# Kernel tuning notes

Hardware: AMD Instinct MI355X
Metric: run time of the kernel (lower is better)

## Reference

```python
import jax, jax.numpy as jnp
import numpy as np

NUM_POINT = 9
BASE_SCALE = 8.0
STRIDE = 8.0


def setup_inputs() -> dict:
    key = jax.random.key(0)
    k1, k2, k3 = jax.random.split(key, 3)
    B, C, H, W = 2, 256, 100, 100
    N = H * W
    feat_map = jax.random.normal(k1, (B, C, H, W), dtype=jnp.float32)
    # grid of location centers (x, y, stride) like the anchor/center generator
    ys, xs = jnp.meshgrid(jnp.arange(H, dtype=jnp.float32), jnp.arange(W, dtype=jnp.float32), indexing='ij')
    cx = (xs.reshape(-1) + 0.5) * STRIDE
    cy = (ys.reshape(-1) + 0.5) * STRIDE
    locations = jnp.stack([cx, cy, jnp.full((N,), STRIDE, dtype=jnp.float32)], axis=-1)
    offset = jax.random.normal(k2, (B, N, NUM_POINT, 2), dtype=jnp.float32) * 2.0
    loc_pred = jax.random.normal(k3, (B, N, NUM_POINT * 2), dtype=jnp.float32)
    return {"feat_map": feat_map, "locations": locations, "offset": offset, "loc_pred": loc_pred}


def bilinear_gather(feat, index):
    # feat: [C, H, W]; index: [P, 2] as (w, h) coords. Returns [C, P].
    H, W = feat.shape[1], feat.shape[2]
    w, h = index[:, 0], index[:, 1]
    h_low = jnp.clip(jnp.floor(h), 0.0, H - 1)
    h_high = jnp.where(h_low >= H - 1, h_low, h_low + 1)
    h = jnp.where(h_low >= H - 1, h_low, h)
    w_low = jnp.clip(jnp.floor(w), 0.0, W - 1)
    w_high = jnp.where(w_low >= W - 1, w_low, w_low + 1)
    w = jnp.where(w_low >= W - 1, w_low, w)
    hl = jax.lax.stop_gradient(h_low).astype(jnp.int32)
    wl = jax.lax.stop_gradient(w_low).astype(jnp.int32)
    hh_i = jax.lax.stop_gradient(h_high).astype(jnp.int32)
    wh_i = jax.lax.stop_gradient(w_high).astype(jnp.int32)
    lh = h - h_low
    lw = w - w_low
    hh = 1.0 - lh
    hw = 1.0 - lw
    v1 = feat[:, hl, wl]
    v2 = feat[:, hl, wh_i]
    v3 = feat[:, hh_i, wl]
    v4 = feat[:, hh_i, wh_i]
    return (hh * hw) * v1 + (hh * lw) * v2 + (lh * hw) * v3 + (lh * lw) * v4


def get_deform_feats(feat_map, locations, offset, stride):
    # feat_map [B,C,H,W], locations [N,3], offset [B,N,np,2]
    B = feat_map.shape[0]
    N = locations.shape[0]
    scale_ = stride * BASE_SCALE
    centers = locations[:, :2][None, :, None, :]          # [1,N,1,2]
    index = (centers + offset * scale_ * 0.1) / stride     # [B,N,np,2]
    index = index.reshape(B, -1, 2)                        # [B, N*np, 2]
    gathered = jax.vmap(bilinear_gather)(feat_map, index)  # [B, C, N*np]
    C = gathered.shape[1]
    # 'c (nb np) -> nb np c' per batch
    return gathered.reshape(B, C, N, NUM_POINT).transpose(0, 2, 3, 1)  # [B,N,np,C]


def get_regression_boxes(locations, offset_pred, loc_pred):
    # locations [N,3]; offset_pred [N, np*2]; loc_pred [N, np*2]
    N = locations.shape[0]
    offs = offset_pred.reshape(N, -1, 2)
    centers = locations[:, :2][:, None, :]                 # [N,1,2]
    scale_ = locations[:, 2] * BASE_SCALE                  # [N]
    offset_point = centers + offs * scale_[:, None, None] * 0.1
    lp = loc_pred.reshape(N, NUM_POINT, 2)
    shifts = lp * scale_[:, None, None] * 0.5
    p = offset_point + shifts                              # [N,np,2]
    x_min = jnp.min(p[..., 0], axis=-1)
    y_min = jnp.min(p[..., 1], axis=-1)
    x_max = jnp.max(p[..., 0], axis=-1)
    y_max = jnp.max(p[..., 1], axis=-1)
    return jnp.stack([x_min, y_min, x_max, y_max], axis=-1)  # [N,4]


def reference(feat_map, locations, offset, loc_pred):
    deform_feats = get_deform_feats(feat_map, locations, offset, STRIDE)
    B, N = offset.shape[0], offset.shape[1]
    boxes = jax.vmap(lambda o, l: get_regression_boxes(locations, o, l))(
        offset.reshape(B, N, -1), loc_pred
    )  # [B,N,4]
    return deform_feats, boxes
```

## Files before the change

### kernel.cpp

```cpp
#include <hip/hip_runtime.h>
#include <float.h>

#define BB      2
#define CCH     256
#define HND     100
#define WND     100
#define NPTS    (HND * WND)
#define NPOINT  9
#define NPTOT   (BB * NPTS * NPOINT)
#define NBOX    (BB * NPTS)

#define GATHER_BLOCKS (NPTOT / 8)
#define BOX_BLOCKS    ((NBOX + 255) / 256)

typedef float    f32x4 __attribute__((ext_vector_type(4)));
typedef unsigned u32x2 __attribute__((ext_vector_type(2)));

__device__ __forceinline__ unsigned short f2bf(float f) {
    unsigned u = __float_as_uint(f);
    return (unsigned short)((u + 0x7FFFu + ((u >> 16) & 1u)) >> 16);
}

__global__ __launch_bounds__(256)
void transpose_feat_bf16(const float* __restrict__ in,
                         unsigned short* __restrict__ out) {
    __shared__ float tile[32][33];
    const int b    = blockIdx.z;
    const int col0 = blockIdx.x * 32;
    const int row0 = blockIdx.y * 32;
    const int tx = threadIdx.x, ty = threadIdx.y;
    const float* src = in + (size_t)b * CCH * NPTS;
#pragma unroll
    for (int i = 0; i < 4; ++i) {
        const int c   = row0 + ty + i * 8;
        const int col = col0 + tx;
        if (col < NPTS)
            tile[ty + i * 8][tx] = src[(size_t)c * NPTS + col];
    }
    __syncthreads();
    const int tid     = ty * 32 + tx;
    const int c_quad  = tid & 7;
    const int hw_loc  = tid >> 3;
    const int hw      = col0 + hw_loc;
    if (hw < NPTS) {
        u32x2 v;
        const float f0 = tile[4 * c_quad + 0][hw_loc];
        const float f1 = tile[4 * c_quad + 1][hw_loc];
        const float f2 = tile[4 * c_quad + 2][hw_loc];
        const float f3 = tile[4 * c_quad + 3][hw_loc];
        v.x = (unsigned)f2bf(f0) | ((unsigned)f2bf(f1) << 16);
        v.y = (unsigned)f2bf(f2) | ((unsigned)f2bf(f3) << 16);
        u32x2* dst = (u32x2*)(out + (size_t)b * NPTS * CCH);
        dst[(size_t)hw * (CCH / 4) + (row0 >> 2) + c_quad] = v;
    }
}

struct Bilin {
    int i1, i2, i3, i4;
    float w1, w2, w3, w4;
};

__device__ __forceinline__ Bilin bilin_setup(float w, float h) {
    Bilin r;
    const float h_low = fminf(fmaxf(floorf(h), 0.0f), (float)(HND - 1));
    const float w_low = fminf(fmaxf(floorf(w), 0.0f), (float)(WND - 1));
    const bool  hcap = (h_low >= (float)(HND - 1));
    const bool  wcap = (w_low >= (float)(WND - 1));
    const float h_high = hcap ? h_low : h_low + 1.0f;
    const float w_high = wcap ? w_low : w_low + 1.0f;
    const float he = hcap ? h_low : h;
    const float we = wcap ? w_low : w;
    const int hl  = (int)h_low,  wl  = (int)w_low;
    const int hhi = (int)h_high, whi = (int)w_high;
    const float lh = he - h_low, lw = we - w_low;
    const float hh = 1.0f - lh,  hw = 1.0f - lw;
    r.w1 = hh * hw; r.w2 = hh * lw; r.w3 = lh * hw; r.w4 = lh * lw;
    r.i1 = hl * WND + wl;  r.i2 = hl * WND + whi;
    r.i3 = hhi * WND + wl; r.i4 = hhi * WND + whi;
    return r;
}

__device__ __forceinline__ f32x4 unpack_bf4(u32x2 v) {
    f32x4 f;
    f.x = __uint_as_float(v.x << 16);
    f.y = __uint_as_float(v.x & 0xFFFF0000u);
    f.z = __uint_as_float(v.y << 16);
    f.w = __uint_as_float(v.y & 0xFFFF0000u);
    return f;
}

__global__ __launch_bounds__(256)
void deform_gather_boxes(const unsigned short* __restrict__ feat,
                         const float* __restrict__ locations,
                         const float* __restrict__ offset,
                         const float* __restrict__ loc_pred,
                         float* __restrict__ out_feats,
                         float* __restrict__ out_boxes)
{
    if (blockIdx.x < GATHER_BLOCKS) {
        const int wid  = threadIdx.x >> 6;
        const int lane = threadIdx.x & 63;
        const int p0 = (blockIdx.x * 4 + wid) * 2;
        const int p1 = p0 + 1;

        const int b0 = p0 / (NPTS * NPOINT);
        const int n0 = (p0 - b0 * (NPTS * NPOINT)) / NPOINT;
        const float w0f = (locations[n0 * 3 + 0] + (offset[(size_t)p0 * 2 + 0] * 64.0f) * 0.1f) * 0.125f;
        const float h0f = (locations[n0 * 3 + 1] + (offset[(size_t)p0 * 2 + 1] * 64.0f) * 0.1f) * 0.125f;
        const Bilin s0 = bilin_setup(w0f, h0f);
        const int b1 = p1 / (NPTS * NPOINT);
        const int n1 = (p1 - b1 * (NPTS * NPOINT)) / NPOINT;
        const float w1f = (locations[n1 * 3 + 0] + (offset[(size_t)p1 * 2 + 0] * 64.0f) * 0.1f) * 0.125f;
        const float h1f = (locations[n1 * 3 + 1] + (offset[(size_t)p1 * 2 + 1] * 64.0f) * 0.1f) * 0.125f;
        const Bilin s1 = bilin_setup(w1f, h1f);

        const u32x2* base0 = (const u32x2*)(feat + (size_t)b0 * NPTS * CCH);
        const u32x2* base1 = (const u32x2*)(feat + (size_t)b1 * NPTS * CCH);

        const u32x2 a0  = base0[(size_t)s0.i1 * (CCH / 4) + lane];
        const u32x2 b0v = base0[(size_t)s0.i2 * (CCH / 4) + lane];
        const u32x2 c0  = base0[(size_t)s0.i3 * (CCH / 4) + lane];
        const u32x2 d0  = base0[(size_t)s0.i4 * (CCH / 4) + lane];
        const u32x2 a1  = base1[(size_t)s1.i1 * (CCH / 4) + lane];
        const u32x2 b1v = base1[(size_t)s1.i2 * (CCH / 4) + lane];
        const u32x2 c1  = base1[(size_t)s1.i3 * (CCH / 4) + lane];
        const u32x2 d1  = base1[(size_t)s1.i4 * (CCH / 4) + lane];

        const f32x4 r0 = s0.w1 * unpack_bf4(a0) + s0.w2 * unpack_bf4(b0v)
                       + s0.w3 * unpack_bf4(c0) + s0.w4 * unpack_bf4(d0);
        const f32x4 r1 = s1.w1 * unpack_bf4(a1) + s1.w2 * unpack_bf4(b1v)
                       + s1.w3 * unpack_bf4(c1) + s1.w4 * unpack_bf4(d1);

        __builtin_nontemporal_store(r0, (f32x4*)(out_feats + (size_t)p0 * CCH) + lane);
        __builtin_nontemporal_store(r1, (f32x4*)(out_feats + (size_t)p1 * CCH) + lane);
    } else {
        const int idx = (blockIdx.x - GATHER_BLOCKS) * 256 + threadIdx.x;
        if (idx >= NBOX) return;
        const int n = idx % NPTS;

        const float cx = locations[n * 3 + 0];
        const float cy = locations[n * 3 + 1];
        const float scale_ = locations[n * 3 + 2] * 8.0f;

        const float* off = offset   + (size_t)idx * (NPOINT * 2);
        const float* lp  = loc_pred + (size_t)idx * (NPOINT * 2);

        float xmin = FLT_MAX, ymin = FLT_MAX, xmax = -FLT_MAX, ymax = -FLT_MAX;
#pragma unroll
        for (int k = 0; k < NPOINT; ++k) {
            const float px = (cx + (off[2 * k    ] * scale_) * 0.1f) + (lp[2 * k    ] * scale_) * 0.5f;
            const float py = (cy + (off[2 * k + 1] * scale_) * 0.1f) + (lp[2 * k + 1] * scale_) * 0.5f;
            xmin = fminf(xmin, px); xmax = fmaxf(xmax, px);
            ymin = fminf(ymin, py); ymax = fmaxf(ymax, py);
        }
        f32x4 bx = { xmin, ymin, xmax, ymax };
        __builtin_nontemporal_store(bx, (f32x4*)(out_boxes + (size_t)idx * 4));
    }
}

__global__ __launch_bounds__(256)
void deform_gather_direct(const float* __restrict__ feat,
                          const float* __restrict__ locations,
                          const float* __restrict__ offset,
                          float* __restrict__ out)
{
    const int wid  = threadIdx.x >> 6;
    const int lane = threadIdx.x & 63;
    const int pid  = blockIdx.x * 4 + wid;
    if (pid >= NPTOT) return;
    const int b   = pid / (NPTS * NPOINT);
    const int n   = (pid - b * (NPTS * NPOINT)) / NPOINT;
    const float w = (locations[n * 3 + 0] + (offset[(size_t)pid * 2 + 0] * 64.0f) * 0.1f) * 0.125f;
    const float h = (locations[n * 3 + 1] + (offset[(size_t)pid * 2 + 1] * 64.0f) * 0.1f) * 0.125f;
    const Bilin s = bilin_setup(w, h);
    const float* base = feat + (size_t)b * CCH * NPTS;
    float* o = out + (size_t)pid * CCH;
    for (int c = lane; c < CCH; c += 64) {
        const float* f = base + (size_t)c * NPTS;
        o[c] = s.w1 * f[s.i1] + s.w2 * f[s.i2] + s.w3 * f[s.i3] + s.w4 * f[s.i4];
    }
}

__global__ __launch_bounds__(256)
void boxes_kernel(const float* __restrict__ locations,
                  const float* __restrict__ offset,
                  const float* __restrict__ loc_pred,
                  float* __restrict__ out)
{
    const int idx = blockIdx.x * blockDim.x + threadIdx.x;
    if (idx >= NBOX) return;
    const int n = idx % NPTS;
    const float cx = locations[n * 3 + 0];
    const float cy = locations[n * 3 + 1];
    const float scale_ = locations[n * 3 + 2] * 8.0f;
    const float* off = offset   + (size_t)idx * (NPOINT * 2);
    const float* lp  = loc_pred + (size_t)idx * (NPOINT * 2);
    float xmin = FLT_MAX, ymin = FLT_MAX, xmax = -FLT_MAX, ymax = -FLT_MAX;
#pragma unroll
    for (int k = 0; k < NPOINT; ++k) {
        const float px = (cx + (off[2 * k    ] * scale_) * 0.1f) + (lp[2 * k    ] * scale_) * 0.5f;
        const float py = (cy + (off[2 * k + 1] * scale_) * 0.1f) + (lp[2 * k + 1] * scale_) * 0.5f;
        xmin = fminf(xmin, px); xmax = fmaxf(xmax, px);
        ymin = fminf(ymin, py); ymax = fmaxf(ymax, py);
    }
    float* ob = out + (size_t)idx * 4;
    ob[0] = xmin; ob[1] = ymin; ob[2] = xmax; ob[3] = ymax;
}

extern "C" void kernel_launch(void* const* d_in, const int* in_sizes, int n_in,
                              void* d_out, int out_size, void* d_ws, size_t ws_size,
                              hipStream_t stream) {
    const float* feat      = (const float*)d_in[0];
    const float* locations = (const float*)d_in[1];
    const float* offset    = (const float*)d_in[2];
    const float* loc_pred  = (const float*)d_in[3];
    float* out = (float*)d_out;

    const size_t deform_elems = (size_t)NPTOT * CCH;
    const size_t need_ws = (size_t)BB * NPTS * CCH * sizeof(unsigned short);

    if (ws_size >= need_ws) {
        dim3 tg((NPTS + 31) / 32, CCH / 32, BB);
        transpose_feat_bf16<<<tg, dim3(32, 8), 0, stream>>>(
            feat, (unsigned short*)d_ws);
        deform_gather_boxes<<<GATHER_BLOCKS + BOX_BLOCKS, 256, 0, stream>>>(
            (const unsigned short*)d_ws, locations, offset, loc_pred,
            out, out + deform_elems);
    } else {
        deform_gather_direct<<<(NPTOT + 3) / 4, 256, 0, stream>>>(
            feat, locations, offset, out);
        boxes_kernel<<<(NBOX + 255) / 256, 256, 0, stream>>>(
            locations, offset, loc_pred, out + deform_elems);
    }
}
```

Baseline: 51.93 us.

## Fuse transpose, boxes and gather into one cooperative persistent kernel with grid sync

Replaces the two-launch sequence (transpose to bf16 and then gather plus boxes) with a single cooperative kernel of 1024 persistent blocks. Phase one grid-strides over the transpose tiles and the box work, a grid-wide sync follows, and phase two grid-strides over the gather. The aim is to remove the second launch and the inter-kernel gap. The cost is a grid barrier, fixed occupancy (launch_bounds 256,4), and loop overhead in place of a one-to-one block mapping. The old two-kernel path is kept as a fallback if the cooperative launch fails.

```diff
diff --git a/kernel.cpp b/kernel.cpp
--- a/kernel.cpp
+++ b/kernel.cpp
@@ -1,5 +1,8 @@
 #include <hip/hip_runtime.h>
+#include <hip/hip_cooperative_groups.h>
 #include <float.h>
+
+namespace cg = cooperative_groups;
 
 #define BB      2
 #define CCH     256
@@ -10,8 +13,12 @@
 #define NPTOT   (BB * NPTS * NPOINT)
 #define NBOX    (BB * NPTS)
 
-#define GATHER_BLOCKS (NPTOT / 8)
-#define BOX_BLOCKS    ((NBOX + 255) / 256)
+#define TP_BX     ((NPTS + 31) / 32)
+#define TP_VB     (TP_BX * (CCH / 32) * BB)
+#define BOX_VB    ((NBOX + 255) / 256)
+#define PH1_VB    (TP_VB + BOX_VB)
+#define GATHER_VB (NPTOT / 8)
+#define COOP_BLOCKS 1024
 
 typedef float    f32x4 __attribute__((ext_vector_type(4)));
 typedef unsigned u32x2 __attribute__((ext_vector_type(2)));
@@ -19,6 +26,152 @@
 __device__ __forceinline__ unsigned short f2bf(float f) {
     unsigned u = __float_as_uint(f);
     return (unsigned short)((u + 0x7FFFu + ((u >> 16) & 1u)) >> 16);
+}
+
+struct Bilin {
+    int i1, i2, i3, i4;
+    float w1, w2, w3, w4;
+};
+
+__device__ __forceinline__ Bilin bilin_setup(float w, float h) {
+    Bilin r;
+    const float h_low = fminf(fmaxf(floorf(h), 0.0f), (float)(HND - 1));
+    const float w_low = fminf(fmaxf(floorf(w), 0.0f), (float)(WND - 1));
+    const bool  hcap = (h_low >= (float)(HND - 1));
+    const bool  wcap = (w_low >= (float)(WND - 1));
+    const float he = hcap ? h_low : h;
+    const float we = wcap ? w_low : w;
+    const int hl  = (int)h_low,  wl  = (int)w_low;
+    const int hhi = hcap ? hl : hl + 1;
+    const int whi = wcap ? wl : wl + 1;
+    const float lh = he - h_low, lw = we - w_low;
+    const float hh = 1.0f - lh,  hw = 1.0f - lw;
+    r.w1 = hh * hw; r.w2 = hh * lw; r.w3 = lh * hw; r.w4 = lh * lw;
+    r.i1 = hl * WND + wl;  r.i2 = hl * WND + whi;
+    r.i3 = hhi * WND + wl; r.i4 = hhi * WND + whi;
+    return r;
+}
+
+__device__ __forceinline__ f32x4 unpack_bf4(u32x2 v) {
+    f32x4 f;
+    f.x = __uint_as_float(v.x << 16);
+    f.y = __uint_as_float(v.x & 0xFFFF0000u);
+    f.z = __uint_as_float(v.y << 16);
+    f.w = __uint_as_float(v.y & 0xFFFF0000u);
+    return f;
+}
+
+__device__ __forceinline__ void boxes_work(int idx,
+                                           const float* __restrict__ locations,
+                                           const float* __restrict__ offset,
+                                           const float* __restrict__ loc_pred,
+                                           float* __restrict__ out_boxes) {
+    if (idx >= NBOX) return;
+    const int n = idx % NPTS;
+    const float cx = locations[n * 3 + 0];
+    const float cy = locations[n * 3 + 1];
+    const float scale_ = locations[n * 3 + 2] * 8.0f;
+    const float* off = offset   + (size_t)idx * (NPOINT * 2);
+    const float* lp  = loc_pred + (size_t)idx * (NPOINT * 2);
+    float xmin = FLT_MAX, ymin = FLT_MAX, xmax = -FLT_MAX, ymax = -FLT_MAX;
+#pragma unroll
+    for (int k = 0; k < NPOINT; ++k) {
+        const float px = (cx + (off[2 * k    ] * scale_) * 0.1f) + (lp[2 * k    ] * scale_) * 0.5f;
+        const float py = (cy + (off[2 * k + 1] * scale_) * 0.1f) + (lp[2 * k + 1] * scale_) * 0.5f;
+        xmin = fminf(xmin, px); xmax = fmaxf(xmax, px);
+        ymin = fminf(ymin, py); ymax = fmaxf(ymax, py);
+    }
+    f32x4 bx = { xmin, ymin, xmax, ymax };
+    __builtin_nontemporal_store(bx, (f32x4*)(out_boxes + (size_t)idx * 4));
+}
+
+__global__ __launch_bounds__(256, 4)
+void fused_all(const float* __restrict__ feat_in,
+               unsigned short* __restrict__ featT,
+               const float* __restrict__ locations,
+               const float* __restrict__ offset,
+               const float* __restrict__ loc_pred,
+               float* __restrict__ out_feats,
+               float* __restrict__ out_boxes)
+{
+    __shared__ float tile[32][33];
+    const int tid = threadIdx.x;
+
+    for (int v = blockIdx.x; v < PH1_VB; v += gridDim.x) {
+        if (v < TP_VB) {
+            const int bz  = v / (TP_BX * (CCH / 32));
+            const int rem = v % (TP_BX * (CCH / 32));
+            const int by  = rem / TP_BX;
+            const int bx  = rem % TP_BX;
+            const int tx = tid & 31, ty = tid >> 5;
+            const float* src = feat_in + (size_t)bz * CCH * NPTS;
+#pragma unroll
+            for (int i = 0; i < 4; ++i) {
+                const int c   = by * 32 + ty + i * 8;
+                const int col = bx * 32 + tx;
+                if (col < NPTS)
+                    tile[ty + i * 8][tx] = src[(size_t)c * NPTS + col];
+            }
+            __syncthreads();
+            const int c_quad = tid & 7;
+            const int hw_loc = tid >> 3;
+            const int hw     = bx * 32 + hw_loc;
+            if (hw < NPTS) {
+                u32x2 pk;
+                const float f0 = tile[4 * c_quad + 0][hw_loc];
+                const float f1 = tile[4 * c_quad + 1][hw_loc];
+                const float f2 = tile[4 * c_quad + 2][hw_loc];
+                const float f3 = tile[4 * c_quad + 3][hw_loc];
+                pk.x = (unsigned)f2bf(f0) | ((unsigned)f2bf(f1) << 16);
+                pk.y = (unsigned)f2bf(f2) | ((unsigned)f2bf(f3) << 16);
+                u32x2* dst = (u32x2*)(featT + (size_t)bz * NPTS * CCH);
+                dst[(size_t)hw * (CCH / 4) + by * 8 + c_quad] = pk;
+            }
+            __syncthreads();
+        } else {
+            boxes_work((v - TP_VB) * 256 + tid, locations, offset, loc_pred, out_boxes);
+        }
+    }
+
+    cg::this_grid().sync();
+
+    const int wid  = tid >> 6;
+    const int lane = tid & 63;
+    for (int v = blockIdx.x; v < GATHER_VB; v += gridDim.x) {
+        const int p0 = (v * 4 + wid) * 2;
+        const int p1 = p0 + 1;
+
+        const int b0 = p0 / (NPTS * NPOINT);
+        const int n0 = (p0 - b0 * (NPTS * NPOINT)) / NPOINT;
+        const float w0f = (locations[n0 * 3 + 0] + (offset[(size_t)p0 * 2 + 0] * 64.0f) * 0.1f) * 0.125f;
+        const float h0f = (locations[n0 * 3 + 1] + (offset[(size_t)p0 * 2 + 1] * 64.0f) * 0.1f) * 0.125f;
+        const Bilin s0 = bilin_setup(w0f, h0f);
+        const int b1 = p1 / (NPTS * NPOINT);
+        const int n1 = (p1 - b1 * (NPTS * NPOINT)) / NPOINT;
+        const float w1f = (locations[n1 * 3 + 0] + (offset[(size_t)p1 * 2 + 0] * 64.0f) * 0.1f) * 0.125f;
+        const float h1f = (locations[n1 * 3 + 1] + (offset[(size_t)p1 * 2 + 1] * 64.0f) * 0.1f) * 0.125f;
+        const Bilin s1 = bilin_setup(w1f, h1f);
+
+        const u32x2* base0 = (const u32x2*)(featT + (size_t)b0 * NPTS * CCH);
+        const u32x2* base1 = (const u32x2*)(featT + (size_t)b1 * NPTS * CCH);
+
+        const u32x2 a0  = base0[(size_t)s0.i1 * (CCH / 4) + lane];
+        const u32x2 b0v = base0[(size_t)s0.i2 * (CCH / 4) + lane];
+        const u32x2 c0  = base0[(size_t)s0.i3 * (CCH / 4) + lane];
+        const u32x2 d0  = base0[(size_t)s0.i4 * (CCH / 4) + lane];
+        const u32x2 a1  = base1[(size_t)s1.i1 * (CCH / 4) + lane];
+        const u32x2 b1v = base1[(size_t)s1.i2 * (CCH / 4) + lane];
+        const u32x2 c1  = base1[(size_t)s1.i3 * (CCH / 4) + lane];
+        const u32x2 d1  = base1[(size_t)s1.i4 * (CCH / 4) + lane];
+
+        const f32x4 r0 = s0.w1 * unpack_bf4(a0) + s0.w2 * unpack_bf4(b0v)
+                       + s0.w3 * unpack_bf4(c0) + s0.w4 * unpack_bf4(d0);
+        const f32x4 r1 = s1.w1 * unpack_bf4(a1) + s1.w2 * unpack_bf4(b1v)
+                       + s1.w3 * unpack_bf4(c1) + s1.w4 * unpack_bf4(d1);
+
+        __builtin_nontemporal_store(r0, (f32x4*)(out_feats + (size_t)p0 * CCH) + lane);
+        __builtin_nontemporal_store(r1, (f32x4*)(out_feats + (size_t)p1 * CCH) + lane);
+    }
 }
 
 __global__ __launch_bounds__(256)
@@ -38,10 +191,10 @@
             tile[ty + i * 8][tx] = src[(size_t)c * NPTS + col];
     }
     __syncthreads();
-    const int tid     = ty * 32 + tx;
-    const int c_quad  = tid & 7;
-    const int hw_loc  = tid >> 3;
-    const int hw      = col0 + hw_loc;
+    const int tid    = ty * 32 + tx;
+    const int c_quad = tid & 7;
+    const int hw_loc = tid >> 3;
+    const int hw     = col0 + hw_loc;
     if (hw < NPTS) {
         u32x2 v;
         const float f0 = tile[4 * c_quad + 0][hw_loc];
@@ -55,40 +208,6 @@
     }
 }
 
-struct Bilin {
-    int i1, i2, i3, i4;
-    float w1, w2, w3, w4;
-};
-
-__device__ __forceinline__ Bilin bilin_setup(float w, float h) {
-    Bilin r;
-    const float h_low = fminf(fmaxf(floorf(h), 0.0f), (float)(HND - 1));
-    const float w_low = fminf(fmaxf(floorf(w), 0.0f), (float)(WND - 1));
-    const bool  hcap = (h_low >= (float)(HND - 1));
-    const bool  wcap = (w_low >= (float)(WND - 1));
-    const float h_high = hcap ? h_low : h_low + 1.0f;
-    const float w_high = wcap ? w_low : w_low + 1.0f;
-    const float he = hcap ? h_low : h;
-    const float we = wcap ? w_low : w;
-    const int hl  = (int)h_low,  wl  = (int)w_low;
-    const int hhi = (int)h_high, whi = (int)w_high;
-    const float lh = he - h_low, lw = we - w_low;
-    const float hh = 1.0f - lh,  hw = 1.0f - lw;
-    r.w1 = hh * hw; r.w2 = hh * lw; r.w3 = lh * hw; r.w4 = lh * lw;
-    r.i1 = hl * WND + wl;  r.i2 = hl * WND + whi;
-    r.i3 = hhi * WND + wl; r.i4 = hhi * WND + whi;
-    return r;
-}
-
-__device__ __forceinline__ f32x4 unpack_bf4(u32x2 v) {
-    f32x4 f;
-    f.x = __uint_as_float(v.x << 16);
-    f.y = __uint_as_float(v.x & 0xFFFF0000u);
-    f.z = __uint_as_float(v.y << 16);
-    f.w = __uint_as_float(v.y & 0xFFFF0000u);
-    return f;
-}
-
 __global__ __launch_bounds__(256)
 void deform_gather_boxes(const unsigned short* __restrict__ feat,
                          const float* __restrict__ locations,
@@ -97,12 +216,11 @@
                          float* __restrict__ out_feats,
                          float* __restrict__ out_boxes)
 {
-    if (blockIdx.x < GATHER_BLOCKS) {
+    if (blockIdx.x < GATHER_VB) {
         const int wid  = threadIdx.x >> 6;
         const int lane = threadIdx.x & 63;
-        const int p0 = (blockIdx.x * 4 + wid) * 2;
+        const int p0 = ((int)blockIdx.x * 4 + wid) * 2;
         const int p1 = p0 + 1;
-
         const int b0 = p0 / (NPTS * NPOINT);
         const int n0 = (p0 - b0 * (NPTS * NPOINT)) / NPOINT;
         const float w0f = (locations[n0 * 3 + 0] + (offset[(size_t)p0 * 2 + 0] * 64.0f) * 0.1f) * 0.125f;
@@ -113,10 +231,8 @@
         const float w1f = (locations[n1 * 3 + 0] + (offset[(size_t)p1 * 2 + 0] * 64.0f) * 0.1f) * 0.125f;
         const float h1f = (locations[n1 * 3 + 1] + (offset[(size_t)p1 * 2 + 1] * 64.0f) * 0.1f) * 0.125f;
         const Bilin s1 = bilin_setup(w1f, h1f);
-
         const u32x2* base0 = (const u32x2*)(feat + (size_t)b0 * NPTS * CCH);
         const u32x2* base1 = (const u32x2*)(feat + (size_t)b1 * NPTS * CCH);
-
         const u32x2 a0  = base0[(size_t)s0.i1 * (CCH / 4) + lane];
         const u32x2 b0v = base0[(size_t)s0.i2 * (CCH / 4) + lane];
         const u32x2 c0  = base0[(size_t)s0.i3 * (CCH / 4) + lane];
@@ -125,36 +241,15 @@
         const u32x2 b1v = base1[(size_t)s1.i2 * (CCH / 4) + lane];
         const u32x2 c1  = base1[(size_t)s1.i3 * (CCH / 4) + lane];
         const u32x2 d1  = base1[(size_t)s1.i4 * (CCH / 4) + lane];
-
         const f32x4 r0 = s0.w1 * unpack_bf4(a0) + s0.w2 * unpack_bf4(b0v)
                        + s0.w3 * unpack_bf4(c0) + s0.w4 * unpack_bf4(d0);
         const f32x4 r1 = s1.w1 * unpack_bf4(a1) + s1.w2 * unpack_bf4(b1v)
                        + s1.w3 * unpack_bf4(c1) + s1.w4 * unpack_bf4(d1);
-
         __builtin_nontemporal_store(r0, (f32x4*)(out_feats + (size_t)p0 * CCH) + lane);
         __builtin_nontemporal_store(r1, (f32x4*)(out_feats + (size_t)p1 * CCH) + lane);
     } else {
-        const int idx = (blockIdx.x - GATHER_BLOCKS) * 256 + threadIdx.x;
-        if (idx >= NBOX) return;
-        const int n = idx % NPTS;
-
-        const float cx = locations[n * 3 + 0];
-        const float cy = locations[n * 3 + 1];
-        const float scale_ = locations[n * 3 + 2] * 8.0f;
-
-        const float* off = offset   + (size_t)idx * (NPOINT * 2);
-        const float* lp  = loc_pred + (size_t)idx * (NPOINT * 2);
-
-        float xmin = FLT_MAX, ymin = FLT_MAX, xmax = -FLT_MAX, ymax = -FLT_MAX;
-#pragma unroll
-        for (int k = 0; k < NPOINT; ++k) {
-            const float px = (cx + (off[2 * k    ] * scale_) * 0.1f) + (lp[2 * k    ] * scale_) * 0.5f;
-            const float py = (cy + (off[2 * k + 1] * scale_) * 0.1f) + (lp[2 * k + 1] * scale_) * 0.5f;
-            xmin = fminf(xmin, px); xmax = fmaxf(xmax, px);
-            ymin = fminf(ymin, py); ymax = fmaxf(ymax, py);
-        }
-        f32x4 bx = { xmin, ymin, xmax, ymax };
-        __builtin_nontemporal_store(bx, (f32x4*)(out_boxes + (size_t)idx * 4));
+        boxes_work(((int)blockIdx.x - GATHER_VB) * 256 + threadIdx.x,
+                   locations, offset, loc_pred, out_boxes);
     }
 }
 
@@ -187,24 +282,7 @@
                   const float* __restrict__ loc_pred,
                   float* __restrict__ out)
 {
-    const int idx = blockIdx.x * blockDim.x + threadIdx.x;
-    if (idx >= NBOX) return;
-    const int n = idx % NPTS;
-    const float cx = locations[n * 3 + 0];
-    const float cy = locations[n * 3 + 1];
-    const float scale_ = locations[n * 3 + 2] * 8.0f;
-    const float* off = offset   + (size_t)idx * (NPOINT * 2);
-    const float* lp  = loc_pred + (size_t)idx * (NPOINT * 2);
-    float xmin = FLT_MAX, ymin = FLT_MAX, xmax = -FLT_MAX, ymax = -FLT_MAX;
-#pragma unroll
-    for (int k = 0; k < NPOINT; ++k) {
-        const float px = (cx + (off[2 * k    ] * scale_) * 0.1f) + (lp[2 * k    ] * scale_) * 0.5f;
-        const float py = (cy + (off[2 * k + 1] * scale_) * 0.1f) + (lp[2 * k + 1] * scale_) * 0.5f;
-        xmin = fminf(xmin, px); xmax = fmaxf(xmax, px);
-        ymin = fminf(ymin, py); ymax = fmaxf(ymax, py);
-    }
-    float* ob = out + (size_t)idx * 4;
-    ob[0] = xmin; ob[1] = ymin; ob[2] = xmax; ob[3] = ymax;
+    boxes_work(blockIdx.x * blockDim.x + threadIdx.x, locations, offset, loc_pred, out);
 }
 
 extern "C" void kernel_launch(void* const* d_in, const int* in_sizes, int n_in,
@@ -220,12 +298,21 @@
     const size_t need_ws = (size_t)BB * NPTS * CCH * sizeof(unsigned short);
 
     if (ws_size >= need_ws) {
-        dim3 tg((NPTS + 31) / 32, CCH / 32, BB);
-        transpose_feat_bf16<<<tg, dim3(32, 8), 0, stream>>>(
-            feat, (unsigned short*)d_ws);
-        deform_gather_boxes<<<GATHER_BLOCKS + BOX_BLOCKS, 256, 0, stream>>>(
-            (const unsigned short*)d_ws, locations, offset, loc_pred,
-            out, out + deform_elems);
+        unsigned short* featT = (unsigned short*)d_ws;
+        float* out_feats = out;
+        float* out_boxes = out + deform_elems;
+        void* args[] = { (void*)&feat, (void*)&featT, (void*)&locations,
+                         (void*)&offset, (void*)&loc_pred,
+                         (void*)&out_feats, (void*)&out_boxes };
+        hipError_t e = hipLaunchCooperativeKernel(
+            reinterpret_cast<const void*>(&fused_all),
+            dim3(COOP_BLOCKS), dim3(256), args, 0, stream);
+        if (e != hipSuccess) {
+            dim3 tg(TP_BX, CCH / 32, BB);
+            transpose_feat_bf16<<<tg, dim3(32, 8), 0, stream>>>(feat, featT);
+            deform_gather_boxes<<<GATHER_VB + BOX_VB, 256, 0, stream>>>(
+                featT, locations, offset, loc_pred, out_feats, out_boxes);
+        }
     } else {
         deform_gather_direct<<<(NPTOT + 3) / 4, 256, 0, stream>>>(
             feat, locations, offset, out);
```

Result: slower. 198.1 us (+281.5%).
